# Kernel optimization log

Measured on AMD Instinct MI355X. Metric: run time of the kernel, lower is better.

Reference implementation:

```python
import jax, jax.numpy as jnp
import numpy as np

EPS = 1e-12  # matches torch F.normalize eps


def _l2_normalize(x, axis=-1):
    # torch.F.normalize: x / max(||x||, eps)
    n = jnp.sqrt(jnp.sum(x * x, axis=axis, keepdims=True))
    return x / jnp.maximum(n, EPS)


def setup_inputs() -> dict:
    N, n_classes, embed_dim = 32768, 1000, 1024
    key = jax.random.key(0)
    k_feat, k_lab, k_proto = jax.random.split(key, 3)

    features = jax.random.normal(k_feat, (N, embed_dim), dtype=jnp.float32)

    # one-hot float labels, as expected by `torch.matmul(labels, self.mean_class)`
    y = jax.random.randint(k_lab, (N,), 0, n_classes)
    labels = jax.nn.one_hot(y, n_classes, dtype=jnp.float32)

    # predefined prototypes: orthonormal rows (ortho_group.rvs equivalent via QR)
    g = jax.random.normal(k_proto, (embed_dim, embed_dim), dtype=jnp.float32)
    q, _ = jnp.linalg.qr(g)
    mean_class = q[:n_classes]  # [n_classes, embed_dim], orthonormal rows

    return {"features": features, "labels": labels, "mean_class": mean_class}


def reference(features, labels, mean_class):
    # features: [N, D]; labels: [N, C] one-hot; mean_class: [C, D]
    # (3-D feature mean-pooling branch not exercised: inputs are 2-D)
    proto_y = labels @ mean_class                 # [N, D]
    f = _l2_normalize(features, axis=1)
    p = _l2_normalize(proto_y, axis=1)
    # diag(f @ p.T) == rowwise dot product -> same math, O(N*D) not O(N^2*D)
    cos = jnp.einsum("nd,nd->n", f, p)            # [N]
    return jnp.mean(1.0 - cos)
```

## Files before the change

kernel.cpp:

```cpp
#include <hip/hip_runtime.h>

constexpr int N_CLASSES = 1000;
constexpr int EMBED     = 1024;

typedef float floatx4 __attribute__((ext_vector_type(4)));

__device__ __forceinline__ floatx4 ntload(const floatx4* p) {
    return __builtin_nontemporal_load(p);
}

__global__ __launch_bounds__(256, 8) void label_scan_kernel(
    const float* __restrict__ labels,
    int* __restrict__ cls_arr, int n_rows)
{
    const int tid  = threadIdx.x;
    const int lane = tid & 63;
    const int wave_id = (blockIdx.x * blockDim.x + tid) >> 6;
    const int n_waves = (gridDim.x * blockDim.x) >> 6;

    const float wb = (float)(4 * lane + 1);
    const floatx4 w0 = {wb,          wb + 1.f,   wb + 2.f,   wb + 3.f};
    const floatx4 w1 = {wb + 256.f,  wb + 257.f, wb + 258.f, wb + 259.f};
    const floatx4 w2 = {wb + 512.f,  wb + 513.f, wb + 514.f, wb + 515.f};
    const floatx4 w3 = {wb + 768.f,  wb + 769.f, wb + 770.f, wb + 771.f};

    for (int r = wave_id; r < n_rows; r += n_waves) {
        const floatx4* lr = (const floatx4*)(labels + (size_t)r * N_CLASSES);
        floatx4 l0 = ntload(lr + lane);
        floatx4 l1 = ntload(lr + lane + 64);
        floatx4 l2 = ntload(lr + lane + 128);
        floatx4 l3 = (lane < N_CLASSES / 4 - 192) ? ntload(lr + lane + 192)
                                                  : (floatx4){0.f, 0.f, 0.f, 0.f};
        float c = l0.x*w0.x + l0.y*w0.y + l0.z*w0.z + l0.w*w0.w;
        c += l1.x*w1.x + l1.y*w1.y + l1.z*w1.z + l1.w*w1.w;
        c += l2.x*w2.x + l2.y*w2.y + l2.z*w2.z + l2.w*w2.w;
        c += l3.x*w3.x + l3.y*w3.y + l3.z*w3.z + l3.w*w3.w;
        unsigned long long m = __ballot(c != 0.0f);
        float cf = __shfl(c, __ffsll(m) - 1, 64);
        if (lane == 0) cls_arr[r] = (int)cf - 1;
    }
}

__global__ __launch_bounds__(256, 8) void feature_dot_kernel(
    const float* __restrict__ features,
    const float* __restrict__ mean_class,
    const int* __restrict__ cls_arr,
    float* __restrict__ partials, int n_rows)
{
    const int tid  = threadIdx.x;
    const int lane = tid & 63;
    const int wave = tid >> 6;
    const int wave_id = (blockIdx.x * blockDim.x + tid) >> 6;
    const int n_waves = (gridDim.x * blockDim.x) >> 6;

    float acc = 0.0f;

    int r = wave_id;
    int cls_cur = (r < n_rows) ? cls_arr[r] : 0;

    for (; r < n_rows; r += n_waves) {
        const int rn = r + n_waves;

        const floatx4* fr = (const floatx4*)(features + (size_t)r * EMBED);
        floatx4 f0 = ntload(fr + lane);
        floatx4 f1 = ntload(fr + lane + 64);
        floatx4 f2 = ntload(fr + lane + 128);
        floatx4 f3 = ntload(fr + lane + 192);

        const int c = __builtin_amdgcn_readfirstlane(cls_cur);
        const floatx4* pr = (const floatx4*)(mean_class + (size_t)c * EMBED);
        floatx4 p0 = pr[lane];
        floatx4 p1 = pr[lane + 64];
        floatx4 p2 = pr[lane + 128];
        floatx4 p3 = pr[lane + 192];

        int cls_nxt = (rn < n_rows) ? cls_arr[rn] : 0;

        float ff = 0.f, pp = 0.f, fp = 0.f;
        ff += f0.x*f0.x + f0.y*f0.y + f0.z*f0.z + f0.w*f0.w;
        pp += p0.x*p0.x + p0.y*p0.y + p0.z*p0.z + p0.w*p0.w;
        fp += f0.x*p0.x + f0.y*p0.y + f0.z*p0.z + f0.w*p0.w;
        ff += f1.x*f1.x + f1.y*f1.y + f1.z*f1.z + f1.w*f1.w;
        pp += p1.x*p1.x + p1.y*p1.y + p1.z*p1.z + p1.w*p1.w;
        fp += f1.x*p1.x + f1.y*p1.y + f1.z*p1.z + f1.w*p1.w;
        ff += f2.x*f2.x + f2.y*f2.y + f2.z*f2.z + f2.w*f2.w;
        pp += p2.x*p2.x + p2.y*p2.y + p2.z*p2.z + p2.w*p2.w;
        fp += f2.x*p2.x + f2.y*p2.y + f2.z*p2.z + f2.w*p2.w;
        ff += f3.x*f3.x + f3.y*f3.y + f3.z*f3.z + f3.w*f3.w;
        pp += p3.x*p3.x + p3.y*p3.y + p3.z*p3.z + p3.w*p3.w;
        fp += f3.x*p3.x + f3.y*p3.y + f3.z*p3.z + f3.w*p3.w;
        #pragma unroll
        for (int msk = 1; msk < 64; msk <<= 1) {
            ff += __shfl_xor(ff, msk, 64);
            pp += __shfl_xor(pp, msk, 64);
            fp += __shfl_xor(fp, msk, 64);
        }
        acc += 1.0f - fp * __builtin_amdgcn_rsqf(fmaxf(ff * pp, 1e-24f));

        cls_cur = cls_nxt;
    }

    __shared__ float s_red[4];
    if (lane == 0) s_red[wave] = acc;
    __syncthreads();
    if (tid == 0)
        partials[blockIdx.x] = s_red[0] + s_red[1] + s_red[2] + s_red[3];
}

__global__ __launch_bounds__(256) void reduce_partials_kernel(
    const float* __restrict__ partials, int num_partials,
    float* __restrict__ out, float inv_n)
{
    const int tid  = threadIdx.x;
    const int lane = tid & 63;
    const int wave = tid >> 6;
    __shared__ float s_red[4];

    float acc = 0.0f;
    for (int i = tid; i < num_partials; i += 256)
        acc += partials[i];
    #pragma unroll
    for (int msk = 1; msk < 64; msk <<= 1)
        acc += __shfl_xor(acc, msk, 64);
    if (lane == 0) s_red[wave] = acc;
    __syncthreads();
    if (tid == 0)
        out[0] = (s_red[0] + s_red[1] + s_red[2] + s_red[3]) * inv_n;
}

extern "C" void kernel_launch(void* const* d_in, const int* in_sizes, int n_in,
                              void* d_out, int out_size, void* d_ws, size_t ws_size,
                              hipStream_t stream) {
    const float* features   = (const float*)d_in[0];
    const float* labels     = (const float*)d_in[1];
    const float* mean_class = (const float*)d_in[2];
    float* out = (float*)d_out;

    float* partials = (float*)d_ws;
    int*   cls_arr  = (int*)((char*)d_ws + 16384);

    const int n_rows = in_sizes[0] / EMBED;
    const int num_blocks = 2048;

    label_scan_kernel<<<num_blocks, 256, 0, stream>>>(labels, cls_arr, n_rows);
    feature_dot_kernel<<<num_blocks, 256, 0, stream>>>(
        features, mean_class, cls_arr, partials, n_rows);
    reduce_partials_kernel<<<1, 256, 0, stream>>>(
        partials, num_blocks, out, 1.0f / (float)n_rows);
}
```

Baseline: 258.9 us.

## Fuse label scan into dot kernel with early-exit chunked one-hot search

Merges the label-scanning kernel into the feature/prototype dot kernel, so the class index no longer goes through a workspace array or a separate launch. The one-hot label row is now scanned in 256-class chunks, and the loop stops at the first chunk holding a nonzero value, which skips reading the remaining label chunks. The grid is halved and the occupancy hint lowered. The price is a serial dependency inside each row (label load, then class index, then prototype load) and less concurrency to hide that latency.

```diff
diff --git a/kernel.cpp b/kernel.cpp
--- a/kernel.cpp
+++ b/kernel.cpp
@@ -9,43 +9,12 @@
     return __builtin_nontemporal_load(p);
 }
 
-__global__ __launch_bounds__(256, 8) void label_scan_kernel(
+__global__ __launch_bounds__(256, 4) void angular_fused_kernel(
+    const float* __restrict__ features,
     const float* __restrict__ labels,
-    int* __restrict__ cls_arr, int n_rows)
-{
-    const int tid  = threadIdx.x;
-    const int lane = tid & 63;
-    const int wave_id = (blockIdx.x * blockDim.x + tid) >> 6;
-    const int n_waves = (gridDim.x * blockDim.x) >> 6;
-
-    const float wb = (float)(4 * lane + 1);
-    const floatx4 w0 = {wb,          wb + 1.f,   wb + 2.f,   wb + 3.f};
-    const floatx4 w1 = {wb + 256.f,  wb + 257.f, wb + 258.f, wb + 259.f};
-    const floatx4 w2 = {wb + 512.f,  wb + 513.f, wb + 514.f, wb + 515.f};
-    const floatx4 w3 = {wb + 768.f,  wb + 769.f, wb + 770.f, wb + 771.f};
-
-    for (int r = wave_id; r < n_rows; r += n_waves) {
-        const floatx4* lr = (const floatx4*)(labels + (size_t)r * N_CLASSES);
-        floatx4 l0 = ntload(lr + lane);
-        floatx4 l1 = ntload(lr + lane + 64);
-        floatx4 l2 = ntload(lr + lane + 128);
-        floatx4 l3 = (lane < N_CLASSES / 4 - 192) ? ntload(lr + lane + 192)
-                                                  : (floatx4){0.f, 0.f, 0.f, 0.f};
-        float c = l0.x*w0.x + l0.y*w0.y + l0.z*w0.z + l0.w*w0.w;
-        c += l1.x*w1.x + l1.y*w1.y + l1.z*w1.z + l1.w*w1.w;
-        c += l2.x*w2.x + l2.y*w2.y + l2.z*w2.z + l2.w*w2.w;
-        c += l3.x*w3.x + l3.y*w3.y + l3.z*w3.z + l3.w*w3.w;
-        unsigned long long m = __ballot(c != 0.0f);
-        float cf = __shfl(c, __ffsll(m) - 1, 64);
-        if (lane == 0) cls_arr[r] = (int)cf - 1;
-    }
-}
-
-__global__ __launch_bounds__(256, 8) void feature_dot_kernel(
-    const float* __restrict__ features,
     const float* __restrict__ mean_class,
-    const int* __restrict__ cls_arr,
-    float* __restrict__ partials, int n_rows)
+    float* __restrict__ partials,
+    int n_rows)
 {
     const int tid  = threadIdx.x;
     const int lane = tid & 63;
@@ -53,28 +22,45 @@
     const int wave_id = (blockIdx.x * blockDim.x + tid) >> 6;
     const int n_waves = (gridDim.x * blockDim.x) >> 6;
 
+    const float wb0 = (float)(4 * lane + 1);
+
     float acc = 0.0f;
 
-    int r = wave_id;
-    int cls_cur = (r < n_rows) ? cls_arr[r] : 0;
-
-    for (; r < n_rows; r += n_waves) {
-        const int rn = r + n_waves;
-
+    for (int r = wave_id; r < n_rows; r += n_waves) {
         const floatx4* fr = (const floatx4*)(features + (size_t)r * EMBED);
         floatx4 f0 = ntload(fr + lane);
         floatx4 f1 = ntload(fr + lane + 64);
         floatx4 f2 = ntload(fr + lane + 128);
         floatx4 f3 = ntload(fr + lane + 192);
 
-        const int c = __builtin_amdgcn_readfirstlane(cls_cur);
-        const floatx4* pr = (const floatx4*)(mean_class + (size_t)c * EMBED);
+        const floatx4* lr = (const floatx4*)(labels + (size_t)r * N_CLASSES);
+        int cls = 0;
+        #pragma unroll
+        for (int ch = 0; ch < 4; ++ch) {
+            floatx4 l;
+            if (ch < 3) {
+                l = ntload(lr + lane + 64 * ch);
+            } else {
+                l = (lane < N_CLASSES / 4 - 192) ? ntload(lr + lane + 192)
+                                                 : (floatx4){0.f, 0.f, 0.f, 0.f};
+            }
+            const float base = wb0 + 256.0f * ch;
+            float c = l.x * base + l.y * (base + 1.0f)
+                    + l.z * (base + 2.0f) + l.w * (base + 3.0f);
+            unsigned long long m = __ballot(c != 0.0f);
+            if (m) {
+                float cf = __shfl(c, __ffsll(m) - 1, 64);
+                cls = (int)cf - 1;
+                break;
+            }
+        }
+        cls = __builtin_amdgcn_readfirstlane(cls);
+
+        const floatx4* pr = (const floatx4*)(mean_class + (size_t)cls * EMBED);
         floatx4 p0 = pr[lane];
         floatx4 p1 = pr[lane + 64];
         floatx4 p2 = pr[lane + 128];
         floatx4 p3 = pr[lane + 192];
-
-        int cls_nxt = (rn < n_rows) ? cls_arr[rn] : 0;
 
         float ff = 0.f, pp = 0.f, fp = 0.f;
         ff += f0.x*f0.x + f0.y*f0.y + f0.z*f0.z + f0.w*f0.w;
@@ -96,8 +82,6 @@
             fp += __shfl_xor(fp, msk, 64);
         }
         acc += 1.0f - fp * __builtin_amdgcn_rsqf(fmaxf(ff * pp, 1e-24f));
-
-        cls_cur = cls_nxt;
     }
 
     __shared__ float s_red[4];
@@ -135,16 +119,13 @@
     const float* labels     = (const float*)d_in[1];
     const float* mean_class = (const float*)d_in[2];
     float* out = (float*)d_out;
-
     float* partials = (float*)d_ws;
-    int*   cls_arr  = (int*)((char*)d_ws + 16384);
 
     const int n_rows = in_sizes[0] / EMBED;
-    const int num_blocks = 2048;
+    const int num_blocks = 1024;
 
-    label_scan_kernel<<<num_blocks, 256, 0, stream>>>(labels, cls_arr, n_rows);
-    feature_dot_kernel<<<num_blocks, 256, 0, stream>>>(
-        features, mean_class, cls_arr, partials, n_rows);
+    angular_fused_kernel<<<num_blocks, 256, 0, stream>>>(
+        features, labels, mean_class, partials, n_rows);
     reduce_partials_kernel<<<1, 256, 0, stream>>>(
         partials, num_blocks, out, 1.0f / (float)n_rows);
 }
```

Result: faster. 249.8 us (-3.5%).
